# Kernel optimization log

Measured on AMD Instinct MI355X. Metric: run time of the kernel, lower is better.

## Reference

```python
import jax, jax.numpy as jnp
import numpy as np

N_HEAD = 16

def setup_inputs() -> dict:
    key = jax.random.key(0)
    k1, k2, k3, k4, k5 = jax.random.split(key, 5)
    B, S, D = 2, 2048, 1024
    return {
        "hidden_states": jax.random.normal(k1, (B, S, D), jnp.float32),
        "w_attn": jax.random.normal(k2, (D, 3 * D), jnp.float32) * 0.02,
        "b_attn": jax.random.normal(k3, (3 * D,), jnp.float32) * 0.02,
        "w_proj": jax.random.normal(k4, (D, D), jnp.float32) * 0.02,
        "b_proj": jax.random.normal(k5, (D,), jnp.float32) * 0.02,
    }

def reference(hidden_states, w_attn, b_attn, w_proj, b_proj):
    B, S, D = hidden_states.shape
    H = N_HEAD
    Dh = D // H
    qkv = hidden_states @ w_attn + b_attn              # [B,S,3D]
    q, k, v = jnp.split(qkv, 3, axis=-1)
    def split_heads(x):
        return x.reshape(B, S, H, Dh).transpose(0, 2, 1, 3)  # [B,H,S,Dh]
    q, k, v = split_heads(q), split_heads(k), split_heads(v)
    # scale=True: divide by sqrt(head_dim) (v.size(-1))
    scores = jnp.einsum("bhqd,bhkd->bhqk", q, k) / jnp.sqrt(jnp.float32(Dh))
    attn = jax.nn.softmax(scores, axis=-1)             # [B,H,S,S]
    out = jnp.einsum("bhqk,bhkd->bhqd", attn, v)       # [B,H,S,Dh]
    out = out.transpose(0, 2, 1, 3).reshape(B, S, D)   # merge heads
    return out @ w_proj + b_proj
```

## Files before the change

kernel.cpp:

```cpp
#include <hip/hip_runtime.h>
#include <hip/hip_bf16.h>

typedef __attribute__((ext_vector_type(8))) short bf16x8;
typedef __attribute__((ext_vector_type(4))) float f32x4;
typedef __attribute__((ext_vector_type(16))) float f32x16;

#define LOG2E 1.4426950408889634f

__device__ inline unsigned short f2bf(float f) {
  union { float f; unsigned u; } x; x.f = f;
  unsigned u = x.u;
  unsigned r = u + 0x7FFFu + ((u >> 16) & 1u);
  return (unsigned short)(r >> 16);
}

__device__ inline unsigned cvtpk(float lo, float hi) {
  unsigned r;
  asm("v_cvt_pk_bf16_f32 %0, %1, %2" : "=v"(r) : "v"(lo), "v"(hi));
  return r;
}

__device__ inline void gload16(const unsigned short* g, unsigned short* l) {
  __builtin_amdgcn_global_load_lds(
      (const __attribute__((address_space(1))) unsigned int*)g,
      (__attribute__((address_space(3))) unsigned int*)l, 16, 0, 0);
}

template <int J>
__device__ inline bf16x8 pack_pfrag(f32x16 p) {
  int X, Y, Z, W;
  asm("v_cvt_pk_bf16_f32 %0, %1, %2" : "=v"(X) : "v"(p[J + 0]), "v"(p[J + 1]));
  asm("v_cvt_pk_bf16_f32 %0, %1, %2" : "=v"(Y) : "v"(p[J + 2]), "v"(p[J + 3]));
  asm("v_cvt_pk_bf16_f32 %0, %1, %2" : "=v"(Z) : "v"(p[J + 4]), "v"(p[J + 5]));
  asm("v_cvt_pk_bf16_f32 %0, %1, %2" : "=v"(W) : "v"(p[J + 6]), "v"(p[J + 7]));
  asm("v_permlane32_swap_b32 %0, %1" : "+v"(X), "+v"(Z));
  asm("v_permlane32_swap_b32 %0, %1" : "+v"(Y), "+v"(W));
  union { int w[4]; bf16x8 v; } u;
  u.w[0] = X; u.w[1] = Y; u.w[2] = Z; u.w[3] = W;
  return u.v;
}

__global__ __launch_bounds__(256) void cvt_bf16(const float* __restrict__ X,
                                                unsigned short* __restrict__ Y, int n4) {
  int i = blockIdx.x * blockDim.x + threadIdx.x;
  int stride = gridDim.x * blockDim.x;
  for (; i < n4; i += stride) {
    float4 v = reinterpret_cast<const float4*>(X)[i];
    ushort4 o;
    o.x = f2bf(v.x); o.y = f2bf(v.y); o.z = f2bf(v.z); o.w = f2bf(v.w);
    reinterpret_cast<ushort4*>(Y)[i] = o;
  }
}

__global__ __launch_bounds__(256) void transpose_cvt(const float* __restrict__ W,
                                                     unsigned short* __restrict__ WT,
                                                     int K, int N) {
  __shared__ unsigned short Tl[64][72];
  const int t = threadIdx.x;
  const int n0 = blockIdx.x * 64, k0 = blockIdx.y * 64;
#pragma unroll
  for (int i = 0; i < 4; ++i) {
    int idx = t + i * 256;
    int r = idx >> 4, c4 = (idx & 15) << 2;
    float4 v = *reinterpret_cast<const float4*>(&W[(size_t)(k0 + r) * N + n0 + c4]);
    Tl[c4 + 0][r] = f2bf(v.x);
    Tl[c4 + 1][r] = f2bf(v.y);
    Tl[c4 + 2][r] = f2bf(v.z);
    Tl[c4 + 3][r] = f2bf(v.w);
  }
  __syncthreads();
#pragma unroll
  for (int i = 0; i < 2; ++i) {
    int idx = t + i * 256;
    int rr = idx >> 3, cc = (idx & 7) << 3;
    *reinterpret_cast<int4*>(&WT[(size_t)(n0 + rr) * K + k0 + cc]) =
        *reinterpret_cast<const int4*>(&Tl[rr][cc]);
  }
}

__global__ __launch_bounds__(512, 2) void gemm_qkv_8p(
    const unsigned short* __restrict__ A, const unsigned short* __restrict__ Bt,
    const float* __restrict__ bias,
    unsigned short* __restrict__ qw, unsigned short* __restrict__ kw,
    unsigned short* __restrict__ vtg) {
  __shared__ unsigned short Abuf[2][16384];
  __shared__ unsigned short Bbuf[2][16384];
  const int t = threadIdx.x, lane = t & 63, wid = t >> 6;
  const int wm = wid >> 2, wn = wid & 3;
  const int orig = blockIdx.x;
  const int nid = (orig & 7) * 24 + (orig >> 3);
  const int mt = nid / 12, nt = nid % 12;
  const int row0 = mt * 256, col0 = nt * 256;
  const int lr = lane & 15, kq = lane >> 4;
  const int srow_lo = lane >> 3;
  const int scg = (lane & 7) ^ srow_lo;
  const unsigned short* Ab = A + (size_t)row0 * 1024;
  const unsigned short* Bb = Bt + (size_t)col0 * 1024;
  f32x4 acc[8][4] = {};

#define SA8(bs, kt)                                                              \
  {                                                                              \
    const unsigned short* Ap = Ab + (kt) * 64;                                   \
    _Pragma("unroll") for (int h = 0; h < 2; ++h)                                \
    _Pragma("unroll") for (int i = 0; i < 2; ++i) {                              \
      int rrel = h * 128 + (wid * 2 + i) * 8 + srow_lo;                          \
      gload16(&Ap[(size_t)rrel * 1024 + scg * 8],                                \
              &Abuf[bs][(h * 16 + wid * 2 + i) * 512]);                          \
    }                                                                            \
  }
#define SB8(bs, kt)                                                              \
  {                                                                              \
    const unsigned short* Bp = Bb + (kt) * 64;                                   \
    _Pragma("unroll") for (int h = 0; h < 2; ++h)                                \
    _Pragma("unroll") for (int i = 0; i < 2; ++i) {                              \
      int rrel = h * 128 + (wid * 2 + i) * 8 + srow_lo;                          \
      gload16(&Bp[(size_t)rrel * 1024 + scg * 8],                                \
              &Bbuf[bs][(h * 16 + wid * 2 + i) * 512]);                          \
    }                                                                            \
  }
#define RDA(dst, mh)                                                             \
  _Pragma("unroll") for (int m = 0; m < 4; ++m)                                  \
  _Pragma("unroll") for (int ks = 0; ks < 2; ++ks) {                             \
    int row = wm * 128 + (mh) * 64 + m * 16 + lr;                                \
    dst[m][ks] = *reinterpret_cast<const bf16x8*>(                               \
        &Ac[row * 64 + (((ks * 4 + kq) ^ (lr & 7)) << 3)]);                      \
  }
#define RDB(dst, nh)                                                             \
  _Pragma("unroll") for (int n = 0; n < 2; ++n)                                  \
  _Pragma("unroll") for (int ks = 0; ks < 2; ++ks) {                             \
    int row = wn * 64 + (nh) * 32 + n * 16 + lr;                                 \
    dst[n][ks] = *reinterpret_cast<const bf16x8*>(                               \
        &Bc[row * 64 + (((ks * 4 + kq) ^ (lr & 7)) << 3)]);                      \
  }
#define QMM(mh, nh, afv, bfv)                                                    \
  _Pragma("unroll") for (int m = 0; m < 4; ++m)                                  \
  _Pragma("unroll") for (int n = 0; n < 2; ++n)                                  \
  _Pragma("unroll") for (int ks = 0; ks < 2; ++ks)                               \
    acc[(mh) * 4 + m][(nh) * 2 + n] = __builtin_amdgcn_mfma_f32_16x16x32_bf16(   \
        afv[m][ks], bfv[n][ks], acc[(mh) * 4 + m][(nh) * 2 + n], 0, 0, 0);
#define BAR8 __builtin_amdgcn_s_barrier();

  SA8(0, 0) SB8(0, 0)
  asm volatile("s_waitcnt vmcnt(0)" ::: "memory");
  BAR8
  __builtin_amdgcn_sched_barrier(0);

  for (int kt = 0; kt < 16; ++kt) {
    const int buf = kt & 1;
    const unsigned short* Ac = Abuf[buf];
    const unsigned short* Bc = Bbuf[buf];
    bf16x8 af0[4][2], af1[4][2], bf0[2][2], bf1[2][2];
    RDA(af0, 0) RDB(bf0, 0)
    if (kt < 15) SA8(buf ^ 1, kt + 1)
    BAR8
    __builtin_amdgcn_s_setprio(1); QMM(0, 0, af0, bf0) __builtin_amdgcn_s_setprio(0);
    BAR8
    RDA(af1, 1)
    if (kt < 15) SB8(buf ^ 1, kt + 1)
    BAR8
    __builtin_amdgcn_s_setprio(1); QMM(1, 0, af1, bf0) __builtin_amdgcn_s_setprio(0);
    BAR8
    RDB(bf1, 1)
    BAR8
    __builtin_amdgcn_s_setprio(1); QMM(0, 1, af0, bf1) __builtin_amdgcn_s_setprio(0);
    BAR8
    if (kt < 15) { asm volatile("s_waitcnt vmcnt(0)" ::: "memory"); }
    BAR8
    __builtin_amdgcn_s_setprio(1); QMM(1, 1, af1, bf1) __builtin_amdgcn_s_setprio(0);
    BAR8
    __builtin_amdgcn_sched_barrier(0);
  }
#undef SA8
#undef SB8
#undef RDA
#undef RDB
#undef QMM
#undef BAR8

  const int rbase = (lane >> 4) * 4;
#pragma unroll
  for (int mm = 0; mm < 8; ++mm) {
#pragma unroll
    for (int nn = 0; nn < 4; ++nn) {
      int c = col0 + wn * 64 + nn * 16 + lr;
      int which = c >> 10;
      int d = c & 1023;
      int h = d >> 6, dh = d & 63;
      float bv = bias[c];
      int m0 = row0 + wm * 128 + mm * 16 + rbase;
      int b = m0 >> 11, s0 = m0 & 2047;
      if (which == 2) {
        int kt = s0 >> 6, key0 = s0 & 63;
        ushort4 pv;
        pv.x = f2bf(acc[mm][nn][0] + bv);
        pv.y = f2bf(acc[mm][nn][1] + bv);
        pv.z = f2bf(acc[mm][nn][2] + bv);
        pv.w = f2bf(acc[mm][nn][3] + bv);
        *reinterpret_cast<ushort4*>(
            &vtg[(((size_t)(b * 16 + h) * 32 + kt) * 64 + dh) * 64 + key0]) = pv;
      } else {
        unsigned short* dst = (which == 0) ? qw : kw;
#pragma unroll
        for (int r = 0; r < 4; ++r)
          dst[(((size_t)b * 16 + h) * 2048 + (s0 + r)) * 64 + dh] = f2bf(acc[mm][nn][r] + bv);
      }
    }
  }
}

#define GST(bs, kt)                                                             \
  {                                                                             \
    const unsigned short* Ap = Ab + (kt) * 32;                                  \
    const unsigned short* Bp = Bb + (kt) * 32;                                  \
    _Pragma("unroll") for (int i = 0; i < 2; ++i) {                             \
      int row = i * 64 + wid * 16 + s_r;                                        \
      gload16(&Ap[(size_t)row * 1024 + s_c], &Al[bs][i * 2048 + wid * 512]);    \
      gload16(&Bp[(size_t)row * 1024 + s_c], &Bl[bs][i * 2048 + wid * 512]);    \
    }                                                                           \
  }

#define GBODY(br)                                                               \
  {                                                                             \
    bf16x8 af[4], bfv[4];                                                       \
    _Pragma("unroll") for (int mm = 0; mm < 4; ++mm) {                          \
      int row = wr + mm * 16 + lr;                                              \
      af[mm] = *reinterpret_cast<const bf16x8*>(                                \
          &Al[br][row * 32 + ((kq ^ (lr & 3)) << 3)]);                          \
    }                                                                           \
    _Pragma("unroll") for (int nn = 0; nn < 4; ++nn) {                          \
      int row = wc + nn * 16 + lr;                                              \
      bfv[nn] = *reinterpret_cast<const bf16x8*>(                               \
          &Bl[br][row * 32 + ((kq ^ (lr & 3)) << 3)]);                          \
    }                                                                           \
    _Pragma("unroll") for (int mm = 0; mm < 4; ++mm)                            \
      _Pragma("unroll") for (int nn = 0; nn < 4; ++nn)                          \
        acc[mm][nn] =                                                           \
            __builtin_amdgcn_mfma_f32_16x16x32_bf16(af[mm], bfv[nn],            \
                                                    acc[mm][nn], 0, 0, 0);      \
  }

#define VMC4 asm volatile("s_waitcnt vmcnt(4)" ::: "memory");
#define VMC0 asm volatile("s_waitcnt vmcnt(0)" ::: "memory");
#define BAR __builtin_amdgcn_s_barrier();

__global__ __launch_bounds__(256) void gemm_proj_b(
    const unsigned short* __restrict__ A, const unsigned short* __restrict__ Bt,
    const float* __restrict__ bias, float* __restrict__ out) {
  const int N = 1024;
  __shared__ unsigned short Al[3][4096];
  __shared__ unsigned short Bl[3][4096];
  const int t = threadIdx.x, lane = t & 63, wid = t >> 6;
  const int wr = (wid >> 1) * 64, wc = (wid & 1) * 64;
  const int orig = blockIdx.x + 8 * blockIdx.y;
  const int nid = (orig & 7) * 32 + (orig >> 3);
  const int row0 = (nid >> 3) * 128, col0 = (nid & 7) * 128;
  const int lr = lane & 15, kq = lane >> 4;
  const int s_r = lane >> 2;
  const int s_c = ((lane & 3) ^ (s_r & 3)) * 8;
  const unsigned short* Ab = A + (size_t)row0 * 1024;
  const unsigned short* Bb = Bt + (size_t)col0 * 1024;
  f32x4 acc[4][4] = {};

  GST(0, 0) GST(1, 1)
  VMC4 BAR
  for (int tt = 0; tt < 30; tt += 3) {
    GST(2, tt + 2) GBODY(0) VMC4 BAR
    GST(0, tt + 3) GBODY(1) VMC4 BAR
    GST(1, tt + 4) GBODY(2) VMC4 BAR
  }
  GBODY(0) VMC0 BAR
  GBODY(1)

  const int rbase = (lane >> 4) * 4;
#pragma unroll
  for (int mm = 0; mm < 4; ++mm) {
#pragma unroll
    for (int nn = 0; nn < 4; ++nn) {
      int c = col0 + wc + nn * 16 + lr;
      float bv = bias[c];
#pragma unroll
      for (int r = 0; r < 4; ++r) {
        int m = row0 + wr + mm * 16 + rbase + r;
        out[(size_t)m * N + c] = acc[mm][nn][r] + bv;
      }
    }
  }
}

__global__ __launch_bounds__(512, 4) void attn_kernel(
    const unsigned short* __restrict__ qw, const unsigned short* __restrict__ kw,
    const unsigned short* __restrict__ vtg, unsigned short* __restrict__ ow) {
  __shared__ char smem[65536];
  unsigned short* KV = (unsigned short*)smem;
  unsigned short* Ol = (unsigned short*)smem;
  float* EX = (float*)(smem + 18432);
  const int t = threadIdx.x, lane = t & 63, wid = t >> 6;
  const int half = wid >> 2, wq = wid & 3;
  const int l31 = lane & 31, hi = lane >> 5;
  const int orig = blockIdx.x + 16 * blockIdx.y;
  const int nid = (orig & 7) * 64 + (orig >> 3);
  const int qt = nid & 15, bh = nid >> 4;
  const int b = bh >> 4, h = bh & 15;
  const unsigned short* Qg = qw + (size_t)bh * 2048 * 64;
  const unsigned short* Kg = kw + (size_t)bh * 2048 * 64;
  const unsigned short* Vg = vtg + (size_t)bh * 32 * 4096;
  const int q0 = qt * 128 + wq * 32;
  const float F = 0.125f * LOG2E;
  const float mF = 16.0f * F;

  union { short s[8]; bf16x8 v; } one_u;
#pragma unroll
  for (int i = 0; i < 8; ++i) one_u.s[i] = (short)0x3F80;
  const bf16x8 ones = one_u.v;

  bf16x8 qf[4];
#pragma unroll
  for (int kc = 0; kc < 4; ++kc)
    qf[kc] = *reinterpret_cast<const bf16x8*>(&Qg[(q0 + l31) * 64 + kc * 16 + hi * 8]);

  f32x16 oA = {0,0,0,0,0,0,0,0,0,0,0,0,0,0,0,0};
  f32x16 oB = {0,0,0,0,0,0,0,0,0,0,0,0,0,0,0,0};
  f32x16 lC = {0,0,0,0,0,0,0,0,0,0,0,0,0,0,0,0};

  const int srow_lo = lane >> 3;
  const int scg = (lane & 7) ^ srow_lo;

#define STAGE(buf, kt)                                                              \
  {                                                                                 \
    const unsigned short* Kt = Kg + (size_t)(kt) * 4096;                            \
    const unsigned short* Vs = Vg + (size_t)(kt) * 4096;                            \
    unsigned short* Kl = KV + half * 16384 + (buf) * 8192;                          \
    unsigned short* Vl = Kl + 4096;                                                 \
    _Pragma("unroll") for (int i = 0; i < 2; ++i) {                                 \
      int chunk = wq * 2 + i;                                                       \
      int row = chunk * 8 + srow_lo;                                                \
      gload16(&Kt[row * 64 + scg * 8], &Kl[chunk * 512]);                           \
      gload16(&Vs[row * 64 + scg * 8], &Vl[chunk * 512]);                           \
    }                                                                               \
  }

  const int kt0 = half * 16;
  STAGE(0, kt0)

  for (int it = 0; it < 16; ++it) {
    const int cur = it & 1;
    if (it + 1 < 16) {
      STAGE(cur ^ 1, kt0 + it + 1)
      asm volatile("s_waitcnt vmcnt(4)" ::: "memory");
    } else {
      asm volatile("s_waitcnt vmcnt(0)" ::: "memory");
    }
    __builtin_amdgcn_s_barrier();
    const unsigned short* Kl = KV + half * 16384 + cur * 8192;
    const unsigned short* Vl = Kl + 4096;

    f32x16 sA = {0,0,0,0,0,0,0,0,0,0,0,0,0,0,0,0};
    f32x16 sB = {0,0,0,0,0,0,0,0,0,0,0,0,0,0,0,0};
    __builtin_amdgcn_s_setprio(1);
#pragma unroll
    for (int kc = 0; kc < 4; ++kc) {
      bf16x8 k0f = *reinterpret_cast<const bf16x8*>(
          &Kl[l31 * 64 + (((kc * 2 + hi) ^ (l31 & 7)) << 3)]);
      bf16x8 k1f = *reinterpret_cast<const bf16x8*>(
          &Kl[(32 + l31) * 64 + (((kc * 2 + hi) ^ (l31 & 7)) << 3)]);
      sA = __builtin_amdgcn_mfma_f32_32x32x16_bf16(k0f, qf[kc], sA, 0, 0, 0);
      sB = __builtin_amdgcn_mfma_f32_32x32x16_bf16(k1f, qf[kc], sB, 0, 0, 0);
    }
    __builtin_amdgcn_s_setprio(0);

#pragma unroll
    for (int j = 0; j < 16; ++j) {
      sA[j] = exp2f(sA[j] * F - mF);
      sB[j] = exp2f(sB[j] * F - mF);
    }

    bf16x8 pf0 = pack_pfrag<0>(sA);
    bf16x8 pf1 = pack_pfrag<8>(sA);
    bf16x8 pf2 = pack_pfrag<0>(sB);
    bf16x8 pf3 = pack_pfrag<8>(sB);

    __builtin_amdgcn_s_setprio(1);
#pragma unroll
    for (int c = 0; c < 4; ++c) {
      bf16x8 pf = (c == 0) ? pf0 : (c == 1) ? pf1 : (c == 2) ? pf2 : pf3;
      int g = c * 2 + hi;
      bf16x8 v0f = *reinterpret_cast<const bf16x8*>(
          &Vl[l31 * 64 + ((g ^ (l31 & 7)) << 3)]);
      bf16x8 v1f = *reinterpret_cast<const bf16x8*>(
          &Vl[(32 + l31) * 64 + ((g ^ (l31 & 7)) << 3)]);
      oA = __builtin_amdgcn_mfma_f32_32x32x16_bf16(v0f, pf, oA, 0, 0, 0);
      oB = __builtin_amdgcn_mfma_f32_32x32x16_bf16(v1f, pf, oB, 0, 0, 0);
      lC = __builtin_amdgcn_mfma_f32_32x32x16_bf16(ones, pf, lC, 0, 0, 0);
    }
    __builtin_amdgcn_s_setprio(0);
    __builtin_amdgcn_s_barrier();
  }
#undef STAGE

  __syncthreads();
  if (half == 1) {
    float* e = EX + ((size_t)(wq * 64 + lane)) * 34;
#pragma unroll
    for (int j = 0; j < 16; ++j) { e[j] = oA[j]; e[16 + j] = oB[j]; }
    e[32] = lC[0];
  }
  __syncthreads();
  if (half == 0) {
    const float* e = EX + ((size_t)(wq * 64 + lane)) * 34;
    float linv = 1.0f / (lC[0] + e[32]);
    unsigned short* orow_l = Ol + (wq * 32 + l31) * 72;
#pragma unroll
    for (int g = 0; g < 4; ++g) {
      float a0 = (oA[4 * g + 0] + e[4 * g + 0]) * linv;
      float a1v = (oA[4 * g + 1] + e[4 * g + 1]) * linv;
      float a2v = (oA[4 * g + 2] + e[4 * g + 2]) * linv;
      float a3v = (oA[4 * g + 3] + e[4 * g + 3]) * linv;
      uint2 w0; w0.x = cvtpk(a0, a1v); w0.y = cvtpk(a2v, a3v);
      *reinterpret_cast<uint2*>(&orow_l[8 * g + 4 * hi]) = w0;
      float b0 = (oB[4 * g + 0] + e[16 + 4 * g + 0]) * linv;
      float b1v = (oB[4 * g + 1] + e[16 + 4 * g + 1]) * linv;
      float b2v = (oB[4 * g + 2] + e[16 + 4 * g + 2]) * linv;
      float b3v = (oB[4 * g + 3] + e[16 + 4 * g + 3]) * linv;
      uint2 w1; w1.x = cvtpk(b0, b1v); w1.y = cvtpk(b2v, b3v);
      *reinterpret_cast<uint2*>(&orow_l[32 + 8 * g + 4 * hi]) = w1;
    }
  }
  __syncthreads();
#pragma unroll
  for (int i = 0; i < 2; ++i) {
    int idx = t + i * 512;
    int q = idx >> 3, ch = idx & 7;
    int4 v = *reinterpret_cast<const int4*>(&Ol[q * 72 + ch * 8]);
    *reinterpret_cast<int4*>(
        &ow[(((size_t)b * 2048 + qt * 128 + q) * 16 + h) * 64 + ch * 8]) = v;
  }
}

extern "C" void kernel_launch(void* const* d_in, const int* in_sizes, int n_in,
                              void* d_out, int out_size, void* d_ws, size_t ws_size,
                              hipStream_t stream) {
  const float* hs = (const float*)d_in[0];
  const float* w_attn = (const float*)d_in[1];
  const float* b_attn = (const float*)d_in[2];
  const float* w_proj = (const float*)d_in[3];
  const float* b_proj = (const float*)d_in[4];
  float* out = (float*)d_out;

  const size_t HEAD = (size_t)2 * 16 * 2048 * 64;
  unsigned short* qw = (unsigned short*)d_ws;
  unsigned short* kw = qw + HEAD;
  unsigned short* vtg = kw + HEAD;
  unsigned short* hs_b = vtg + HEAD;
  unsigned short* ow = hs_b;
  unsigned short* wT = hs_b + HEAD;
  unsigned short* pT = wT + (size_t)3072 * 1024;

  cvt_bf16<<<2048, 256, 0, stream>>>(hs, hs_b, 1048576);
  transpose_cvt<<<dim3(48, 16), 256, 0, stream>>>(w_attn, wT, 1024, 3072);
  transpose_cvt<<<dim3(16, 16), 256, 0, stream>>>(w_proj, pT, 1024, 1024);

  gemm_qkv_8p<<<dim3(192), 512, 0, stream>>>(hs_b, wT, b_attn, qw, kw, vtg);
  attn_kernel<<<dim3(16, 32), 512, 0, stream>>>(qw, kw, vtg, ow);
  gemm_proj_b<<<dim3(8, 32), 256, 0, stream>>>(ow, pT, b_proj, out);
}
```

Baseline: 131.7 us.

## Retile QKV GEMM to 256x192 tiles and fold softmax scale into Q

Changes the QKV projection tile from 256x256 to 256x192, so the grid grows from 192 to 256 blocks, one per CU on a 256-CU device. The LDS staging, fragment reads and MFMA groups are reworked for three 16-wide column fragments per wave. The softmax scale times log2(e) is now applied to Q in the GEMM epilogue, which removes a multiply-subtract per score element in the attention inner loop. The fixed offset of 16*F before exp2 is also dropped, which raises the risk of exp2 overflow on large scores.

```diff
diff --git a/kernel.cpp b/kernel.cpp
--- a/kernel.cpp
+++ b/kernel.cpp
@@ -6,6 +6,7 @@
 typedef __attribute__((ext_vector_type(16))) float f32x16;
 
 #define LOG2E 1.4426950408889634f
+#define SCALE_F (0.125f * LOG2E)
 
 __device__ inline unsigned short f2bf(float f) {
   union { float f; unsigned u; } x; x.f = f;
@@ -84,38 +85,36 @@
     unsigned short* __restrict__ qw, unsigned short* __restrict__ kw,
     unsigned short* __restrict__ vtg) {
   __shared__ unsigned short Abuf[2][16384];
-  __shared__ unsigned short Bbuf[2][16384];
+  __shared__ unsigned short Bbuf[2][12288];
   const int t = threadIdx.x, lane = t & 63, wid = t >> 6;
   const int wm = wid >> 2, wn = wid & 3;
   const int orig = blockIdx.x;
-  const int nid = (orig & 7) * 24 + (orig >> 3);
-  const int mt = nid / 12, nt = nid % 12;
-  const int row0 = mt * 256, col0 = nt * 256;
+  const int nid = (orig & 7) * 32 + (orig >> 3);
+  const int mt = nid >> 4, nt = nid & 15;
+  const int row0 = mt * 256, col0 = nt * 192;
   const int lr = lane & 15, kq = lane >> 4;
   const int srow_lo = lane >> 3;
   const int scg = (lane & 7) ^ srow_lo;
   const unsigned short* Ab = A + (size_t)row0 * 1024;
   const unsigned short* Bb = Bt + (size_t)col0 * 1024;
-  f32x4 acc[8][4] = {};
+  f32x4 acc[8][3] = {};
 
 #define SA8(bs, kt)                                                              \
   {                                                                              \
     const unsigned short* Ap = Ab + (kt) * 64;                                   \
-    _Pragma("unroll") for (int h = 0; h < 2; ++h)                                \
-    _Pragma("unroll") for (int i = 0; i < 2; ++i) {                              \
-      int rrel = h * 128 + (wid * 2 + i) * 8 + srow_lo;                          \
-      gload16(&Ap[(size_t)rrel * 1024 + scg * 8],                                \
-              &Abuf[bs][(h * 16 + wid * 2 + i) * 512]);                          \
+    _Pragma("unroll") for (int i = 0; i < 4; ++i) {                              \
+      int g = wid * 4 + i;                                                       \
+      int rrel = g * 8 + srow_lo;                                                \
+      gload16(&Ap[(size_t)rrel * 1024 + scg * 8], &Abuf[bs][g * 512]);           \
     }                                                                            \
   }
 #define SB8(bs, kt)                                                              \
   {                                                                              \
     const unsigned short* Bp = Bb + (kt) * 64;                                   \
-    _Pragma("unroll") for (int h = 0; h < 2; ++h)                                \
-    _Pragma("unroll") for (int i = 0; i < 2; ++i) {                              \
-      int rrel = h * 128 + (wid * 2 + i) * 8 + srow_lo;                          \
-      gload16(&Bp[(size_t)rrel * 1024 + scg * 8],                                \
-              &Bbuf[bs][(h * 16 + wid * 2 + i) * 512]);                          \
+    _Pragma("unroll") for (int i = 0; i < 3; ++i) {                              \
+      int g = wid * 3 + i;                                                       \
+      int rrel = g * 8 + srow_lo;                                                \
+      gload16(&Bp[(size_t)rrel * 1024 + scg * 8], &Bbuf[bs][g * 512]);           \
     }                                                                            \
   }
 #define RDA(dst, mh)                                                             \
@@ -123,21 +122,32 @@
   _Pragma("unroll") for (int ks = 0; ks < 2; ++ks) {                             \
     int row = wm * 128 + (mh) * 64 + m * 16 + lr;                                \
     dst[m][ks] = *reinterpret_cast<const bf16x8*>(                               \
-        &Ac[row * 64 + (((ks * 4 + kq) ^ (lr & 7)) << 3)]);                      \
-  }
-#define RDB(dst, nh)                                                             \
+        &Ac[row * 64 + (((ks * 4 + kq) ^ (row & 7)) << 3)]);                     \
+  }
+#define RDB2(dst)                                                                \
   _Pragma("unroll") for (int n = 0; n < 2; ++n)                                  \
   _Pragma("unroll") for (int ks = 0; ks < 2; ++ks) {                             \
-    int row = wn * 64 + (nh) * 32 + n * 16 + lr;                                 \
+    int row = wn * 48 + n * 16 + lr;                                             \
     dst[n][ks] = *reinterpret_cast<const bf16x8*>(                               \
-        &Bc[row * 64 + (((ks * 4 + kq) ^ (lr & 7)) << 3)]);                      \
-  }
-#define QMM(mh, nh, afv, bfv)                                                    \
+        &Bc[row * 64 + (((ks * 4 + kq) ^ (row & 7)) << 3)]);                     \
+  }
+#define RDB1(dst)                                                                \
+  _Pragma("unroll") for (int ks = 0; ks < 2; ++ks) {                             \
+    int row = wn * 48 + 32 + lr;                                                 \
+    dst[0][ks] = *reinterpret_cast<const bf16x8*>(                               \
+        &Bc[row * 64 + (((ks * 4 + kq) ^ (row & 7)) << 3)]);                     \
+  }
+#define QMM2(mh, afv, bfv)                                                       \
   _Pragma("unroll") for (int m = 0; m < 4; ++m)                                  \
   _Pragma("unroll") for (int n = 0; n < 2; ++n)                                  \
   _Pragma("unroll") for (int ks = 0; ks < 2; ++ks)                               \
-    acc[(mh) * 4 + m][(nh) * 2 + n] = __builtin_amdgcn_mfma_f32_16x16x32_bf16(   \
-        afv[m][ks], bfv[n][ks], acc[(mh) * 4 + m][(nh) * 2 + n], 0, 0, 0);
+    acc[(mh) * 4 + m][n] = __builtin_amdgcn_mfma_f32_16x16x32_bf16(              \
+        afv[m][ks], bfv[n][ks], acc[(mh) * 4 + m][n], 0, 0, 0);
+#define QMM1(mh, afv, bfv)                                                       \
+  _Pragma("unroll") for (int m = 0; m < 4; ++m)                                  \
+  _Pragma("unroll") for (int ks = 0; ks < 2; ++ks)                               \
+    acc[(mh) * 4 + m][2] = __builtin_amdgcn_mfma_f32_16x16x32_bf16(              \
+        afv[m][ks], bfv[0][ks], acc[(mh) * 4 + m][2], 0, 0, 0);
 #define BAR8 __builtin_amdgcn_s_barrier();
 
   SA8(0, 0) SB8(0, 0)
@@ -149,40 +159,42 @@
     const int buf = kt & 1;
     const unsigned short* Ac = Abuf[buf];
     const unsigned short* Bc = Bbuf[buf];
-    bf16x8 af0[4][2], af1[4][2], bf0[2][2], bf1[2][2];
-    RDA(af0, 0) RDB(bf0, 0)
+    bf16x8 af0[4][2], af1[4][2], bf0[2][2], bf1[1][2];
+    RDA(af0, 0) RDB2(bf0)
     if (kt < 15) SA8(buf ^ 1, kt + 1)
     BAR8
-    __builtin_amdgcn_s_setprio(1); QMM(0, 0, af0, bf0) __builtin_amdgcn_s_setprio(0);
+    __builtin_amdgcn_s_setprio(1); QMM2(0, af0, bf0) __builtin_amdgcn_s_setprio(0);
     BAR8
     RDA(af1, 1)
     if (kt < 15) SB8(buf ^ 1, kt + 1)
     BAR8
-    __builtin_amdgcn_s_setprio(1); QMM(1, 0, af1, bf0) __builtin_amdgcn_s_setprio(0);
-    BAR8
-    RDB(bf1, 1)
-    BAR8
-    __builtin_amdgcn_s_setprio(1); QMM(0, 1, af0, bf1) __builtin_amdgcn_s_setprio(0);
+    __builtin_amdgcn_s_setprio(1); QMM2(1, af1, bf0) __builtin_amdgcn_s_setprio(0);
+    BAR8
+    RDB1(bf1)
+    BAR8
+    __builtin_amdgcn_s_setprio(1); QMM1(0, af0, bf1) __builtin_amdgcn_s_setprio(0);
     BAR8
     if (kt < 15) { asm volatile("s_waitcnt vmcnt(0)" ::: "memory"); }
     BAR8
-    __builtin_amdgcn_s_setprio(1); QMM(1, 1, af1, bf1) __builtin_amdgcn_s_setprio(0);
+    __builtin_amdgcn_s_setprio(1); QMM1(1, af1, bf1) __builtin_amdgcn_s_setprio(0);
     BAR8
     __builtin_amdgcn_sched_barrier(0);
   }
 #undef SA8
 #undef SB8
 #undef RDA
-#undef RDB
-#undef QMM
+#undef RDB2
+#undef RDB1
+#undef QMM2
+#undef QMM1
 #undef BAR8
 
   const int rbase = (lane >> 4) * 4;
 #pragma unroll
   for (int mm = 0; mm < 8; ++mm) {
 #pragma unroll
-    for (int nn = 0; nn < 4; ++nn) {
-      int c = col0 + wn * 64 + nn * 16 + lr;
+    for (int nn = 0; nn < 3; ++nn) {
+      int c = col0 + wn * 48 + nn * 16 + lr;
       int which = c >> 10;
       int d = c & 1023;
       int h = d >> 6, dh = d & 63;
@@ -198,11 +210,15 @@
         pv.w = f2bf(acc[mm][nn][3] + bv);
         *reinterpret_cast<ushort4*>(
             &vtg[(((size_t)(b * 16 + h) * 32 + kt) * 64 + dh) * 64 + key0]) = pv;
+      } else if (which == 1) {
+#pragma unroll
+        for (int r = 0; r < 4; ++r)
+          kw[(((size_t)b * 16 + h) * 2048 + (s0 + r)) * 64 + dh] = f2bf(acc[mm][nn][r] + bv);
       } else {
-        unsigned short* dst = (which == 0) ? qw : kw;
 #pragma unroll
         for (int r = 0; r < 4; ++r)
-          dst[(((size_t)b * 16 + h) * 2048 + (s0 + r)) * 64 + dh] = f2bf(acc[mm][nn][r] + bv);
+          qw[(((size_t)b * 16 + h) * 2048 + (s0 + r)) * 64 + dh] =
+              f2bf((acc[mm][nn][r] + bv) * SCALE_F);
       }
     }
   }
@@ -305,8 +321,6 @@
   const unsigned short* Kg = kw + (size_t)bh * 2048 * 64;
   const unsigned short* Vg = vtg + (size_t)bh * 32 * 4096;
   const int q0 = qt * 128 + wq * 32;
-  const float F = 0.125f * LOG2E;
-  const float mF = 16.0f * F;
 
   union { short s[8]; bf16x8 v; } one_u;
 #pragma unroll
@@ -370,8 +384,8 @@
 
 #pragma unroll
     for (int j = 0; j < 16; ++j) {
-      sA[j] = exp2f(sA[j] * F - mF);
-      sB[j] = exp2f(sB[j] * F - mF);
+      sA[j] = exp2f(sA[j]);
+      sB[j] = exp2f(sB[j]);
     }
 
     bf16x8 pf0 = pack_pfrag<0>(sA);
@@ -459,7 +473,7 @@
   transpose_cvt<<<dim3(48, 16), 256, 0, stream>>>(w_attn, wT, 1024, 3072);
   transpose_cvt<<<dim3(16, 16), 256, 0, stream>>>(w_proj, pT, 1024, 1024);
 
-  gemm_qkv_8p<<<dim3(192), 512, 0, stream>>>(hs_b, wT, b_attn, qw, kw, vtg);
+  gemm_qkv_8p<<<dim3(256), 512, 0, stream>>>(hs_b, wT, b_attn, qw, kw, vtg);
   attn_kernel<<<dim3(16, 32), 512, 0, stream>>>(qw, kw, vtg, ow);
   gemm_proj_b<<<dim3(8, 32), 256, 0, stream>>>(ow, pT, b_proj, out);
 }
```

New measurement: 125.1 us. -5.0%, faster.
